# Performance work log

Measured on AMD Instinct MI355X. Metric: run time of the kernel, lower is better.

Reference implementation:

```python
import jax, jax.numpy as jnp
import numpy as np

N_NODES = 50000
N_EDGES = 1600000
IN_DIM = 64 + 2 + 64   # protein + spatial + lri
HID = 64
OUT_DIM = 32
NUM_GRAPHS = 64
NEG_SLOPE = 0.2  # PyG GATConv default negative_slope


def _gat(x, src, dst, W, a_src, a_dst, bias):
    """PyG-style GATConv: x' = xW per head, per-edge attention with
    LeakyReLU + scatter-softmax over incoming edges, weighted scatter-sum.
    Heads are concatenated (concat=True default)."""
    N = x.shape[0]
    H, C = a_src.shape
    xp = (x @ W).reshape(N, H, C)                      # [N,H,C]
    al_src = jnp.sum(xp * a_src, axis=-1)              # [N,H]
    al_dst = jnp.sum(xp * a_dst, axis=-1)              # [N,H]
    e = jax.nn.leaky_relu(al_src[src] + al_dst[dst], NEG_SLOPE)  # [E,H]
    # numerically stable segment softmax over edges grouped by dst
    m = jax.ops.segment_max(e, dst, num_segments=N)
    ex = jnp.exp(e - m[dst])
    denom = jax.ops.segment_sum(ex, dst, num_segments=N)
    alpha = ex / denom[dst]                            # [E,H]
    out = jax.ops.segment_sum(alpha[:, :, None] * xp[src], dst, num_segments=N)
    return out.reshape(N, H * C) + bias


def setup_inputs() -> dict:
    key = jax.random.key(0)
    ks = jax.random.split(key, 16)
    def glorot(k, shape):
        fan_in = shape[0] if len(shape) == 2 else shape[-1]
        return jax.random.normal(k, shape, dtype=jnp.float32) / np.sqrt(fan_in)
    inp = {
        "protein_expr": jax.random.normal(ks[0], (N_NODES, 64), dtype=jnp.float32),
        "spatial_pos": jax.random.uniform(ks[1], (N_NODES, 2), dtype=jnp.float32),
        "lri_feats": jax.random.normal(ks[2], (N_NODES, 64), dtype=jnp.float32),
        "edge_index": jax.random.randint(ks[3], (2, N_EDGES), 0, N_NODES, dtype=jnp.int64),
        "batch": jnp.sort(jax.random.randint(ks[4], (N_NODES,), 0, NUM_GRAPHS, dtype=jnp.int64)),
        # encoder1: GATConv(IN_DIM -> HID, heads=2)
        "W1": glorot(ks[5], (IN_DIM, 2 * HID)),
        "a_src1": glorot(ks[6], (2, HID)),
        "a_dst1": glorot(ks[7], (2, HID)),
        "b1": jnp.zeros((2 * HID,), dtype=jnp.float32),
        # encoder2: GATConv(2*HID -> HID, heads=1)
        "W2": glorot(ks[8], (2 * HID, HID)),
        "a_src2": glorot(ks[9], (1, HID)),
        "a_dst2": glorot(ks[10], (1, HID)),
        "b2": jnp.zeros((HID,), dtype=jnp.float32),
        # decoder MLP
        "Wd1": glorot(ks[11], (HID, HID)),
        "bd1": jnp.zeros((HID,), dtype=jnp.float32),
        "Wd2": glorot(ks[12], (HID, OUT_DIM)),
        "bd2": jnp.zeros((OUT_DIM,), dtype=jnp.float32),
    }
    return inp


def reference(protein_expr, spatial_pos, lri_feats, edge_index, batch,
              W1, a_src1, a_dst1, b1, W2, a_src2, a_dst2, b2,
              Wd1, bd1, Wd2, bd2):
    N = protein_expr.shape[0]
    x = jnp.concatenate([protein_expr, spatial_pos, lri_feats], axis=1)  # [N, IN_DIM]
    # PyG GATConv adds self-loops by default
    loop = jnp.arange(N, dtype=edge_index.dtype)
    src = jnp.concatenate([edge_index[0], loop])
    dst = jnp.concatenate([edge_index[1], loop])
    h = _gat(x, src, dst, W1, a_src1, a_dst1, b1)   # [N, 2*HID]
    h = _gat(h, src, dst, W2, a_src2, a_dst2, b2)   # [N, HID]
    # global_mean_pool
    counts = jax.ops.segment_sum(jnp.ones((N,), h.dtype), batch, num_segments=NUM_GRAPHS)
    pooled = jax.ops.segment_sum(h, batch, num_segments=NUM_GRAPHS) / jnp.clip(counts, 1.0)[:, None]
    # decoder MLP
    d = jax.nn.relu(pooled @ Wd1 + bd1)
    return d @ Wd2 + bd2
```

## Files before the change

### kernel.cpp

```cpp
#include <hip/hip_runtime.h>
#include <hip/hip_bf16.h>

#define N_NODESC 50000
#define N_EDGESC 1600000
#define NUM_GRAPHSC 64
#define SLICE_W 6250
#define BCAP 230000
#define CH_EPB 2048
#define EPB2 8192
#define SUBW 196
#define NSUB 32
#define SBCAP 8192
#define POOL_REP 32
#define AGG_NB 6250

typedef __hip_bfloat16 bf16;
typedef short short8 __attribute__((ext_vector_type(8)));
typedef float floatx4 __attribute__((ext_vector_type(4)));

__device__ __forceinline__ float ldf(const void* p, long i, int fp32) {
    return fp32 ? ((const float*)p)[i] : __bfloat162float(((const bf16*)p)[i]);
}
__device__ __forceinline__ short f2s(float v) {
    bf16 h = __float2bfloat16(v);
    return *(short*)&h;
}
__device__ __forceinline__ unsigned pack2(float lo, float hi) {
    bf16 a = __float2bfloat16(lo), b = __float2bfloat16(hi);
    unsigned ua = *(unsigned short*)&a, ub = *(unsigned short*)&b;
    return (ub << 16) | ua;
}
__device__ __forceinline__ float ulo(unsigned u) { return __uint_as_float(u << 16); }
__device__ __forceinline__ float uhi(unsigned u) { return __uint_as_float(u & 0xffff0000u); }

__global__ void detect_k(const void* __restrict__ prot,
                         const void* __restrict__ eidx,
                         int* __restrict__ flags) {
    if (blockIdx.x == 0 && threadIdx.x == 0) {
        const bf16* pb = (const bf16*)prot;
        int sane = 0;
        for (int i = 0; i < 64; ++i) {
            float a = fabsf(__bfloat162float(pb[2 * i]));
            if (a > 1e-8f && a < 1e4f) sane++;
        }
        flags[0] = (sane >= 48) ? 0 : 1;
        const unsigned* u = (const unsigned*)eidx;
        int zhi = 0;
        for (int i = 0; i < 32; ++i)
            if (u[2 * i + 1] == 0u) zhi++;
        flags[1] = (zhi >= 30) ? 1 : 0;
    }
}

__global__ __launch_bounds__(256) void prep2_k(const void* __restrict__ W1,
                                               const void* __restrict__ W2,
                                               const int* __restrict__ flags,
                                               short* __restrict__ w1f,
                                               float* __restrict__ w1r,
                                               short* __restrict__ w2f,
                                               int* __restrict__ zreg, int nzero, int nzblk,
                                               const void* __restrict__ batch,
                                               int* __restrict__ b32) {
    const int fp32 = flags[0];
    const int b = blockIdx.x, tid = threadIdx.x;
    if (b < 64) {
        int idx = b * 256 + tid;
        int kp = idx >> 7, n = idx & 127;
        int krow = kp < 64 ? kp : 66 + (kp - 64);
        float v = ldf(W1, (long)krow * 128 + n, fp32);
        int c = n >> 4, nn = n & 15, t = kp >> 5, q = (kp >> 3) & 3, j = kp & 7;
        w1f[(((c * 4 + t) * 4 + q) * 16 + nn) * 8 + j] = f2s(v);
    } else if (b == 64) {
        int which = tid >> 7, n = tid & 127;
        w1r[which * 128 + n] = ldf(W1, (long)(64 + which) * 128 + n, fp32);
    } else if (b < 97) {
        int idx = (b - 65) * 256 + tid;
        int k = idx >> 6, n = idx & 63;
        float v = ldf(W2, (long)k * 64 + n, fp32);
        int c = n >> 4, nn = n & 15, t = k >> 5, q = (k >> 3) & 3, j = k & 7;
        w2f[(((c * 4 + t) * 4 + q) * 16 + nn) * 8 + j] = f2s(v);
    } else if (b < 97 + nzblk) {
        int i = (b - 97) * 256 + tid;
        if (i < nzero) zreg[i] = 0;
    } else {
        const int i64f = flags[1];
        int i = (b - 97 - nzblk) * 256 + tid;
        if (i < N_NODESC)
            b32[i] = i64f ? (int)((const long long*)batch)[i] : ((const int*)batch)[i];
    }
}

__global__ __launch_bounds__(256) void cvt_bucket_k(const void* __restrict__ eidx,
                                                    const int* __restrict__ flags,
                                                    int* __restrict__ bcur,
                                                    unsigned* __restrict__ bucket) {
    const int i64f = flags[1];
    const int tid = threadIdx.x;
    const long e0 = (long)blockIdx.x * CH_EPB;
    __shared__ int cnt[9];
    __shared__ int gbase[8];
    __shared__ int cur[8];
    __shared__ unsigned buf[CH_EPB];
    if (tid < 8) cnt[tid] = 0;
    __syncthreads();
    unsigned ev[8];
    int bk[8];
    #pragma unroll
    for (int i = 0; i < 8; ++i) {
        long e = e0 + i * 256 + tid;
        bk[i] = -1;
        if (e < N_EDGESC) {
            int s, d;
            if (i64f) {
                s = (int)((const long long*)eidx)[e];
                d = (int)((const long long*)eidx)[N_EDGESC + e];
            } else {
                s = ((const int*)eidx)[e];
                d = ((const int*)eidx)[N_EDGESC + e];
            }
            int b = d / SLICE_W;
            bk[i] = b;
            ev[i] = (unsigned)s | ((unsigned)(d - b * SLICE_W) << 16);
            atomicAdd(&cnt[b], 1);
        }
    }
    __syncthreads();
    if (tid == 0) {
        int run = 0;
        #pragma unroll
        for (int b = 0; b < 8; ++b) { int c = cnt[b]; cnt[b] = run; run += c; }
        cnt[8] = run;
    }
    __syncthreads();
    if (tid < 8) {
        int c = cnt[tid + 1] - cnt[tid];
        gbase[tid] = c ? atomicAdd(&bcur[tid], c) : 0;
        cur[tid] = cnt[tid];
    }
    __syncthreads();
    #pragma unroll
    for (int i = 0; i < 8; ++i) {
        if (bk[i] >= 0) {
            int p = atomicAdd(&cur[bk[i]], 1);
            buf[p] = ev[i];
        }
    }
    __syncthreads();
    const int total = cnt[8];
    for (int p = tid; p < total; p += 256) {
        int b = 7;
        #pragma unroll
        for (int q = 6; q >= 0; --q)
            if (p < cnt[q + 1]) b = q;
        bucket[(long)b * BCAP + gbase[b] + (p - cnt[b])] = buf[p];
    }
}

__global__ __launch_bounds__(256) void subpart_k(const unsigned* __restrict__ bucket,
                                                 const int* __restrict__ bcur,
                                                 int* __restrict__ scnt,
                                                 unsigned* __restrict__ bucket2) {
    const int slice = blockIdx.x & 7;
    const int blk = blockIdx.x >> 3;
    const int tid = threadIdx.x;
    const int cnt = bcur[slice];
    const unsigned* B = bucket + (long)slice * BCAP;
    __shared__ unsigned buf[EPB2];
    __shared__ int cnt2[NSUB + 1], gbase[NSUB], cur[NSUB];
    for (int start = blk * EPB2; start < cnt; start += 32 * EPB2) {
        const int csize = min(EPB2, cnt - start);
        if (tid < NSUB) cnt2[tid] = 0;
        __syncthreads();
        for (int i = tid; i < csize; i += 256) {
            unsigned v = B[start + i];
            atomicAdd(&cnt2[(v >> 16) / SUBW], 1);
        }
        __syncthreads();
        if (tid == 0) {
            int run = 0;
            #pragma unroll
            for (int s = 0; s < NSUB; ++s) { int c = cnt2[s]; cnt2[s] = run; run += c; }
            cnt2[NSUB] = run;
        }
        __syncthreads();
        if (tid < NSUB) {
            int c = cnt2[tid + 1] - cnt2[tid];
            gbase[tid] = c ? atomicAdd(&scnt[slice * NSUB + tid], c) : 0;
            cur[tid] = cnt2[tid];
        }
        __syncthreads();
        for (int i = tid; i < csize; i += 256) {
            unsigned v = B[start + i];
            int off = (int)(v >> 16);
            int sub = off / SUBW;
            unsigned nv = (v & 0xffffu) | ((unsigned)(off - sub * SUBW) << 16);
            int p = atomicAdd(&cur[sub], 1);
            buf[p] = nv;
        }
        __syncthreads();
        const int total = cnt2[NSUB];
        for (int p = tid; p < total; p += 256) {
            int lo = 0, hi = NSUB;
            while (hi - lo > 1) { int mid = (lo + hi) >> 1; if (p >= cnt2[mid]) lo = mid; else hi = mid; }
            bucket2[((long)slice * NSUB + lo) * SBCAP + gbase[lo] + (p - cnt2[lo])] = buf[p];
        }
        __syncthreads();
    }
}

__global__ __launch_bounds__(256) void csr_k(const unsigned* __restrict__ bucket2,
                                             const int* __restrict__ scnt,
                                             int* __restrict__ state,
                                             int* __restrict__ row_start,
                                             unsigned short* __restrict__ col) {
    const int sb = blockIdx.x;
    const int slice = sb >> 5, sub = sb & 31;
    const int tid = threadIdx.x;
    const int lane = tid & 63;
    const int cnt = scnt[sb];
    const unsigned* B = bucket2 + (long)sb * SBCAP;
    __shared__ int lh[SUBW];
    __shared__ int sc[256];
    __shared__ int sprefix_sh;
    const int width = min(SUBW, SLICE_W - sub * SUBW);
    const int nodebase = slice * SLICE_W + sub * SUBW;
    for (int i = tid; i < SUBW; i += 256) lh[i] = 0;
    __syncthreads();
    for (int e = tid; e < cnt; e += 256) atomicAdd(&lh[B[e] >> 16], 1);
    __syncthreads();
    const int myc = (tid < SUBW) ? lh[tid] : 0;
    sc[tid] = myc;
    __syncthreads();
    for (int off = 1; off < 256; off <<= 1) {
        int t = (tid >= off) ? sc[tid - off] : 0;
        __syncthreads();
        sc[tid] += t;
        __syncthreads();
    }
    const int total = sc[255];
    if (tid == 0)
        __hip_atomic_store(&state[sb], (int)((1u << 30) | (unsigned)total),
                           __ATOMIC_RELEASE, __HIP_MEMORY_SCOPE_AGENT);
    if (tid < 64) {
        int prefix = 0;
        if (sb > 0) {
            int base = sb;
            for (;;) {
                int t = base - 1 - lane;
                int v = 0;
                if (t >= 0) {
                    for (;;) {
                        v = __hip_atomic_load(&state[t], __ATOMIC_ACQUIRE,
                                              __HIP_MEMORY_SCOPE_AGENT);
                        if ((unsigned)v >= (1u << 30)) break;
                        __builtin_amdgcn_s_sleep(1);
                    }
                }
                int flag = (int)(((unsigned)v) >> 30);
                int val = v & 0x3fffffff;
                unsigned long long pmask = __ballot(flag == 2 && t >= 0);
                int stop_tid = pmask ? (__ffsll((long long)pmask) - 1) : 64;
                int contrib = 0;
                if (t >= 0 && lane <= stop_tid) contrib = val;
                #pragma unroll
                for (int off = 32; off; off >>= 1) contrib += __shfl_xor(contrib, off, 64);
                prefix += contrib;
                if (pmask || base <= 64) break;
                base -= 64;
            }
        }
        if (tid == 0) {
            sprefix_sh = prefix;
            __hip_atomic_store(&state[sb],
                               (int)((2u << 30) | (unsigned)(prefix + total)),
                               __ATOMIC_RELEASE, __HIP_MEMORY_SCOPE_AGENT);
        }
    }
    __syncthreads();
    const int sprefix = sprefix_sh;
    if (tid < width) row_start[nodebase + tid] = sprefix + sc[tid] - myc;
    if (sb == 255 && tid == 0) row_start[N_NODESC] = sprefix + total;
    if (tid < SUBW) lh[tid] = sprefix + sc[tid] - myc;
    __syncthreads();
    for (int e = tid; e < cnt; e += 256) {
        unsigned v = B[e];
        int pos = atomicAdd(&lh[v >> 16], 1);
        col[pos] = (unsigned short)(v & 0xffffu);
    }
}


__global__ __launch_bounds__(256) void gemm1_k(
        const void* __restrict__ prot, const void* __restrict__ sp,
        const void* __restrict__ lri,
        const short* __restrict__ w1f, const float* __restrict__ w1r,
        const void* __restrict__ as1, const void* __restrict__ ad1,
        const int* __restrict__ flags,
        short* __restrict__ xph0, short* __restrict__ xph1,
        float* __restrict__ alsrc, float* __restrict__ aldst) {
    const int fp32 = flags[0];
    const int tid = threadIdx.x;
    const int nb = blockIdx.x * 32;
    __shared__ __align__(16) short xs[32][136];
    __shared__ float xsp[32][2];
    __shared__ float sredc[32][8], dredc[32][8];

    if (!fp32) {
        #pragma unroll
        for (int i = 0; i < 2; ++i) {
            int cidx = i * 256 + tid;
            int r = cidx >> 4, cc = cidx & 15;
            int g = nb + r;
            short8 v = (short8){0, 0, 0, 0, 0, 0, 0, 0};
            if (g < N_NODESC) {
                const short* srcp = (cc < 8)
                    ? (const short*)prot + (long)g * 64 + cc * 8
                    : (const short*)lri + (long)g * 64 + (cc - 8) * 8;
                v = *(const short8*)srcp;
            }
            *(short8*)&xs[r][cc * 8] = v;
        }
    } else {
        #pragma unroll
        for (int i = 0; i < 16; ++i) {
            int idx = i * 256 + tid;
            int r = idx >> 7, k = idx & 127;
            int g = nb + r;
            float v = 0.f;
            if (g < N_NODESC)
                v = (k < 64) ? ((const float*)prot)[(long)g * 64 + k]
                             : ((const float*)lri)[(long)g * 64 + (k - 64)];
            xs[r][k] = f2s(v);
        }
    }
    if (tid < 64) {
        int r = tid >> 1, which = tid & 1;
        int g = nb + r;
        xsp[r][which] = (g < N_NODESC) ? ldf(sp, (long)g * 2 + which, fp32) : 0.f;
    }
    __syncthreads();

    const int wid = tid >> 6, lane = tid & 63;
    const int quad = lane >> 4, l16 = lane & 15;
    floatx4 acc[2][2];
    #pragma unroll
    for (int a = 0; a < 2; ++a)
        #pragma unroll
        for (int b = 0; b < 2; ++b) acc[a][b] = (floatx4){0.f, 0.f, 0.f, 0.f};

    const int c0 = 2 * wid;
    #pragma unroll
    for (int t = 0; t < 4; ++t) {
        short8 a0 = *(const short8*)&xs[l16][t * 32 + quad * 8];
        short8 a1 = *(const short8*)&xs[16 + l16][t * 32 + quad * 8];
        short8 b0 = *(const short8*)&w1f[(((c0 * 4 + t) * 4 + quad) * 16 + l16) * 8];
        short8 b1 = *(const short8*)&w1f[((((c0 + 1) * 4 + t) * 4 + quad) * 16 + l16) * 8];
        acc[0][0] = __builtin_amdgcn_mfma_f32_16x16x32_bf16(a0, b0, acc[0][0], 0, 0, 0);
        acc[0][1] = __builtin_amdgcn_mfma_f32_16x16x32_bf16(a0, b1, acc[0][1], 0, 0, 0);
        acc[1][0] = __builtin_amdgcn_mfma_f32_16x16x32_bf16(a1, b0, acc[1][0], 0, 0, 0);
        acc[1][1] = __builtin_amdgcn_mfma_f32_16x16x32_bf16(a1, b1, acc[1][1], 0, 0, 0);
    }
    #pragma unroll
    for (int ci = 0; ci < 2; ++ci) {
        int colg = (c0 + ci) * 16 + l16;
        float w0 = w1r[colg], w1v = w1r[128 + colg];
        float asv = ldf(as1, colg, fp32), adv = ldf(ad1, colg, fp32);
        short* xpd = (colg < 64) ? xph0 : xph1;
        const int cc = colg & 63;
        #pragma unroll
        for (int rt = 0; rt < 2; ++rt) {
            float sv[4], dv[4];
            #pragma unroll
            for (int reg = 0; reg < 4; ++reg) {
                int row = rt * 16 + quad * 4 + reg;
                int g = nb + row;
                float v = acc[rt][ci][reg] + xsp[row][0] * w0 + xsp[row][1] * w1v;
                if (g < N_NODESC) xpd[(long)g * 64 + cc] = f2s(v);
                sv[reg] = v * asv;
                dv[reg] = v * adv;
            }
            #pragma unroll
            for (int off = 1; off < 16; off <<= 1) {
                #pragma unroll
                for (int reg = 0; reg < 4; ++reg) {
                    sv[reg] += __shfl_xor(sv[reg], off, 64);
                    dv[reg] += __shfl_xor(dv[reg], off, 64);
                }
            }
            if (l16 == 0) {
                #pragma unroll
                for (int reg = 0; reg < 4; ++reg) {
                    int row = rt * 16 + quad * 4 + reg;
                    sredc[row][c0 + ci] = sv[reg];
                    dredc[row][c0 + ci] = dv[reg];
                }
            }
        }
    }
    __syncthreads();
    if (tid < 64) {
        int r = tid >> 1, h = tid & 1;
        int g = nb + r;
        if (g < N_NODESC) {
            alsrc[(long)h * N_NODESC + g] = sredc[r][4 * h] + sredc[r][4 * h + 1] +
                                            sredc[r][4 * h + 2] + sredc[r][4 * h + 3];
            aldst[(long)h * N_NODESC + g] = dredc[r][4 * h] + dredc[r][4 * h + 1] +
                                            dredc[r][4 * h + 2] + dredc[r][4 * h + 3];
        }
    }
}


__global__ __launch_bounds__(256) void agg1s_k(
        const int* __restrict__ row_start, const unsigned short* __restrict__ col,
        const short* __restrict__ xph0, const short* __restrict__ xph1,
        const float* __restrict__ als, const float* __restrict__ ald,
        const void* __restrict__ b1, const int* __restrict__ flags,
        unsigned* __restrict__ h1b32) {
    const int fp32 = flags[0];
    const int tid = threadIdx.x;
    const int wid = tid >> 6;
    const int lane = tid & 63;
    const int hw = lane >> 5;
    const int hl = lane & 31;
    const int head = blockIdx.x >= AGG_NB;
    const int b = blockIdx.x - head * AGG_NB;
    const int n = b * 8 + wid * 2 + hw;
    __shared__ float2 pbuf[4][2][32];
    float2* mybuf = pbuf[wid][hw];
    const short* xph = head ? xph1 : xph0;
    const float* alsh = als + (long)head * N_NODESC;
    const float* aldh = ald + (long)head * N_NODESC;
    const int e = hl >> 3;
    const int c = hl & 7;
    const char* xpb = (const char*)xph;
    const int c16 = c * 16;
    const float ad = aldh[n];
    float e0 = alsh[n] + ad;
    e0 = e0 > 0.f ? e0 : 0.2f * e0;
    const float pself = __expf(e0);
    const float pinit = e == 0 ? pself : 0.f;
    uint4 us = *(const uint4*)(xpb + (long)n * 128 + c16);
    float acc0 = pinit * ulo(us.x), acc1 = pinit * uhi(us.x);
    float acc2 = pinit * ulo(us.y), acc3 = pinit * uhi(us.y);
    float acc4 = pinit * ulo(us.z), acc5 = pinit * uhi(us.z);
    float acc6 = pinit * ulo(us.w), acc7 = pinit * uhi(us.w);
    float lp = 0.f;
    const int beg = row_start[n], end = row_start[n + 1];
    for (int base = beg; base < end; base += 32) {
        const int idx = base + hl;
        int s = 0;
        float p = 0.f;
        if (idx < end) {
            s = (int)col[idx];
            float t = alsh[s] + ad;
            t = t > 0.f ? t : 0.2f * t;
            p = __expf(t);
        }
        lp += p;
        mybuf[hl] = make_float2(p, __int_as_float(s << 7));
        int cnt = end - base; if (cnt > 32) cnt = 32;
        int quads = (cnt + 3) >> 2;
        int j = 0;
        for (; j + 4 <= quads; j += 4) {
            int a4[4]; float p4[4]; uint4 x[4];
            #pragma unroll
            for (int q = 0; q < 4; ++q) {
                float2 bv = mybuf[4 * (j + q) + e];
                a4[q] = __float_as_int(bv.y);
                p4[q] = bv.x;
            }
            #pragma unroll
            for (int q = 0; q < 4; ++q)
                x[q] = *(const uint4*)(xpb + a4[q] + c16);
            #pragma unroll
            for (int q = 0; q < 4; ++q) {
                acc0 = fmaf(p4[q], ulo(x[q].x), acc0);
                acc1 = fmaf(p4[q], uhi(x[q].x), acc1);
                acc2 = fmaf(p4[q], ulo(x[q].y), acc2);
                acc3 = fmaf(p4[q], uhi(x[q].y), acc3);
                acc4 = fmaf(p4[q], ulo(x[q].z), acc4);
                acc5 = fmaf(p4[q], uhi(x[q].z), acc5);
                acc6 = fmaf(p4[q], ulo(x[q].w), acc6);
                acc7 = fmaf(p4[q], uhi(x[q].w), acc7);
            }
        }
        for (; j < quads; ++j) {
            float2 bv = mybuf[4 * j + e];
            uint4 x = *(const uint4*)(xpb + __float_as_int(bv.y) + c16);
            float pv = bv.x;
            acc0 = fmaf(pv, ulo(x.x), acc0);
            acc1 = fmaf(pv, uhi(x.x), acc1);
            acc2 = fmaf(pv, ulo(x.y), acc2);
            acc3 = fmaf(pv, uhi(x.y), acc3);
            acc4 = fmaf(pv, ulo(x.z), acc4);
            acc5 = fmaf(pv, uhi(x.z), acc5);
            acc6 = fmaf(pv, ulo(x.w), acc6);
            acc7 = fmaf(pv, uhi(x.w), acc7);
        }
    }
    #pragma unroll
    for (int off = 16; off; off >>= 1) lp += __shfl_xor(lp, off, 64);
    #pragma unroll
    for (int off = 8; off <= 16; off <<= 1) {
        acc0 += __shfl_xor(acc0, off, 64);
        acc1 += __shfl_xor(acc1, off, 64);
        acc2 += __shfl_xor(acc2, off, 64);
        acc3 += __shfl_xor(acc3, off, 64);
        acc4 += __shfl_xor(acc4, off, 64);
        acc5 += __shfl_xor(acc5, off, 64);
        acc6 += __shfl_xor(acc6, off, 64);
        acc7 += __shfl_xor(acc7, off, 64);
    }
    if (hl < 8) {
        const float rl = 1.f / (lp + pself);
        const long bb = (long)head * 64 + 8 * c;
        float o0 = acc0 * rl + ldf(b1, bb + 0, fp32);
        float o1 = acc1 * rl + ldf(b1, bb + 1, fp32);
        float o2 = acc2 * rl + ldf(b1, bb + 2, fp32);
        float o3 = acc3 * rl + ldf(b1, bb + 3, fp32);
        float o4 = acc4 * rl + ldf(b1, bb + 4, fp32);
        float o5 = acc5 * rl + ldf(b1, bb + 5, fp32);
        float o6 = acc6 * rl + ldf(b1, bb + 6, fp32);
        float o7 = acc7 * rl + ldf(b1, bb + 7, fp32);
        uint4 o;
        o.x = pack2(o0, o1); o.y = pack2(o2, o3);
        o.z = pack2(o4, o5); o.w = pack2(o6, o7);
        *(uint4*)((char*)h1b32 + (long)n * 256 + head * 128 + c16) = o;
    }
}


__global__ __launch_bounds__(256) void gemm2_k(
        const unsigned* __restrict__ h1b32, const short* __restrict__ w2f,
        const void* __restrict__ as2, const void* __restrict__ ad2,
        const int* __restrict__ flags,
        short* __restrict__ xp2b, float* __restrict__ alsrc, float* __restrict__ aldst) {
    const int fp32 = flags[0];
    const int tid = threadIdx.x;
    const int nb = blockIdx.x * 32;
    __shared__ __align__(16) short xs[32][136];
    __shared__ float sredc[32][4], dredc[32][4];

    #pragma unroll
    for (int i = 0; i < 8; ++i) {
        int idx = i * 256 + tid;
        int r = idx >> 6, ii = idx & 63;
        int g = nb + r;
        unsigned val = (g < N_NODESC) ? h1b32[(long)g * 64 + ii] : 0u;
        ((unsigned*)&xs[r][0])[ii] = val;
    }
    __syncthreads();

    const int wid = tid >> 6, lane = tid & 63;
    const int quad = lane >> 4, l16 = lane & 15;
    floatx4 acc0 = (floatx4){0.f, 0.f, 0.f, 0.f};
    floatx4 acc1 = (floatx4){0.f, 0.f, 0.f, 0.f};
    #pragma unroll
    for (int t = 0; t < 4; ++t) {
        short8 a0 = *(const short8*)&xs[l16][t * 32 + quad * 8];
        short8 a1 = *(const short8*)&xs[16 + l16][t * 32 + quad * 8];
        short8 b = *(const short8*)&w2f[(((wid * 4 + t) * 4 + quad) * 16 + l16) * 8];
        acc0 = __builtin_amdgcn_mfma_f32_16x16x32_bf16(a0, b, acc0, 0, 0, 0);
        acc1 = __builtin_amdgcn_mfma_f32_16x16x32_bf16(a1, b, acc1, 0, 0, 0);
    }
    const int colg = wid * 16 + l16;
    const float asv = ldf(as2, colg, fp32), adv = ldf(ad2, colg, fp32);
    float sv0[4], dv0[4], sv1[4], dv1[4];
    #pragma unroll
    for (int reg = 0; reg < 4; ++reg) {
        int r0 = quad * 4 + reg;
        int g0 = nb + r0;
        int g1 = g0 + 16;
        if (g0 < N_NODESC) xp2b[(long)g0 * 64 + colg] = f2s(acc0[reg]);
        if (g1 < N_NODESC) xp2b[(long)g1 * 64 + colg] = f2s(acc1[reg]);
        sv0[reg] = acc0[reg] * asv; dv0[reg] = acc0[reg] * adv;
        sv1[reg] = acc1[reg] * asv; dv1[reg] = acc1[reg] * adv;
    }
    #pragma unroll
    for (int off = 1; off < 16; off <<= 1) {
        #pragma unroll
        for (int reg = 0; reg < 4; ++reg) {
            sv0[reg] += __shfl_xor(sv0[reg], off, 64);
            dv0[reg] += __shfl_xor(dv0[reg], off, 64);
            sv1[reg] += __shfl_xor(sv1[reg], off, 64);
            dv1[reg] += __shfl_xor(dv1[reg], off, 64);
        }
    }
    if (l16 == 0) {
        #pragma unroll
        for (int reg = 0; reg < 4; ++reg) {
            int r0 = quad * 4 + reg;
            sredc[r0][wid] = sv0[reg];      dredc[r0][wid] = dv0[reg];
            sredc[r0 + 16][wid] = sv1[reg]; dredc[r0 + 16][wid] = dv1[reg];
        }
    }
    __syncthreads();
    if (tid < 32) {
        int g = nb + tid;
        if (g < N_NODESC) {
            alsrc[g] = sredc[tid][0] + sredc[tid][1] + sredc[tid][2] + sredc[tid][3];
            aldst[g] = dredc[tid][0] + dredc[tid][1] + dredc[tid][2] + dredc[tid][3];
        }
    }
}


__global__ __launch_bounds__(256) void agg2p_k(
        const int* __restrict__ row_start, const unsigned short* __restrict__ col,
        const short* __restrict__ xp2b, const float* __restrict__ alsrc,
        const float* __restrict__ aldst, const void* __restrict__ b2v,
        const int* __restrict__ flags, const int* __restrict__ batch32,
        float* __restrict__ pooled, float* __restrict__ counts) {
    const int fp32 = flags[0];
    const int tid = threadIdx.x;
    const int wid = tid >> 6;
    const int lane = tid & 63;
    const int hw = lane >> 5;
    const int hl = lane & 31;
    const int n = blockIdx.x * 8 + wid * 2 + hw;
    const int rep = blockIdx.x & (POOL_REP - 1);
    __shared__ float2 pbuf[4][2][32];
    __shared__ float psum[64];
    __shared__ int ginfo[2];
    if (tid < 64) psum[tid] = 0.f;
    if (tid == 0) {
        int g0 = batch32[blockIdx.x * 8];
        int g7 = batch32[blockIdx.x * 8 + 7];
        ginfo[0] = g0;
        ginfo[1] = (g0 == g7);
    }
    __syncthreads();
    float2* mybuf = pbuf[wid][hw];
    const int e = hl >> 3;
    const int c = hl & 7;
    const char* xpb = (const char*)xp2b;
    const int c16 = c * 16;
    const float ad = aldst[n];
    float e0 = alsrc[n] + ad;
    e0 = e0 > 0.f ? e0 : 0.2f * e0;
    const float pself = __expf(e0);
    const float pinit = e == 0 ? pself : 0.f;
    uint4 us = *(const uint4*)(xpb + (long)n * 128 + c16);
    float acc0 = pinit * ulo(us.x), acc1 = pinit * uhi(us.x);
    float acc2 = pinit * ulo(us.y), acc3 = pinit * uhi(us.y);
    float acc4 = pinit * ulo(us.z), acc5 = pinit * uhi(us.z);
    float acc6 = pinit * ulo(us.w), acc7 = pinit * uhi(us.w);
    float lp = 0.f;
    const int beg = row_start[n], end = row_start[n + 1];
    for (int base = beg; base < end; base += 32) {
        const int idx = base + hl;
        int s = 0;
        float p = 0.f;
        if (idx < end) {
            s = (int)col[idx];
            float t = alsrc[s] + ad;
            t = t > 0.f ? t : 0.2f * t;
            p = __expf(t);
        }
        lp += p;
        mybuf[hl] = make_float2(p, __int_as_float(s << 7));
        int cnt = end - base; if (cnt > 32) cnt = 32;
        int quads = (cnt + 3) >> 2;
        int j = 0;
        for (; j + 4 <= quads; j += 4) {
            int a4[4]; float p4[4]; uint4 x[4];
            #pragma unroll
            for (int q = 0; q < 4; ++q) {
                float2 bv = mybuf[4 * (j + q) + e];
                a4[q] = __float_as_int(bv.y);
                p4[q] = bv.x;
            }
            #pragma unroll
            for (int q = 0; q < 4; ++q)
                x[q] = *(const uint4*)(xpb + a4[q] + c16);
            #pragma unroll
            for (int q = 0; q < 4; ++q) {
                acc0 = fmaf(p4[q], ulo(x[q].x), acc0);
                acc1 = fmaf(p4[q], uhi(x[q].x), acc1);
                acc2 = fmaf(p4[q], ulo(x[q].y), acc2);
                acc3 = fmaf(p4[q], uhi(x[q].y), acc3);
                acc4 = fmaf(p4[q], ulo(x[q].z), acc4);
                acc5 = fmaf(p4[q], uhi(x[q].z), acc5);
                acc6 = fmaf(p4[q], ulo(x[q].w), acc6);
                acc7 = fmaf(p4[q], uhi(x[q].w), acc7);
            }
        }
        for (; j < quads; ++j) {
            float2 bv = mybuf[4 * j + e];
            uint4 x = *(const uint4*)(xpb + __float_as_int(bv.y) + c16);
            float pv = bv.x;
            acc0 = fmaf(pv, ulo(x.x), acc0);
            acc1 = fmaf(pv, uhi(x.x), acc1);
            acc2 = fmaf(pv, ulo(x.y), acc2);
            acc3 = fmaf(pv, uhi(x.y), acc3);
            acc4 = fmaf(pv, ulo(x.z), acc4);
            acc5 = fmaf(pv, uhi(x.z), acc5);
            acc6 = fmaf(pv, ulo(x.w), acc6);
            acc7 = fmaf(pv, uhi(x.w), acc7);
        }
    }
    #pragma unroll
    for (int off = 16; off; off >>= 1) lp += __shfl_xor(lp, off, 64);
    #pragma unroll
    for (int off = 8; off <= 16; off <<= 1) {
        acc0 += __shfl_xor(acc0, off, 64);
        acc1 += __shfl_xor(acc1, off, 64);
        acc2 += __shfl_xor(acc2, off, 64);
        acc3 += __shfl_xor(acc3, off, 64);
        acc4 += __shfl_xor(acc4, off, 64);
        acc5 += __shfl_xor(acc5, off, 64);
        acc6 += __shfl_xor(acc6, off, 64);
        acc7 += __shfl_xor(acc7, off, 64);
    }
    float o[8];
    if (hl < 8) {
        const float rl = 1.f / (lp + pself);
        o[0] = acc0 * rl + ldf(b2v, 8 * c + 0, fp32);
        o[1] = acc1 * rl + ldf(b2v, 8 * c + 1, fp32);
        o[2] = acc2 * rl + ldf(b2v, 8 * c + 2, fp32);
        o[3] = acc3 * rl + ldf(b2v, 8 * c + 3, fp32);
        o[4] = acc4 * rl + ldf(b2v, 8 * c + 4, fp32);
        o[5] = acc5 * rl + ldf(b2v, 8 * c + 5, fp32);
        o[6] = acc6 * rl + ldf(b2v, 8 * c + 6, fp32);
        o[7] = acc7 * rl + ldf(b2v, 8 * c + 7, fp32);
    }
    if (ginfo[1]) {
        if (hl < 8) {
            #pragma unroll
            for (int j = 0; j < 8; ++j) atomicAdd(&psum[8 * c + j], o[j]);
        }
        __syncthreads();
        if (tid < 64)
            atomicAdd(&pooled[((long)rep * NUM_GRAPHSC + ginfo[0]) * 64 + tid], psum[tid]);
        if (tid == 0) atomicAdd(&counts[rep * NUM_GRAPHSC + ginfo[0]], 8.f);
    } else {
        int g = batch32[n];
        if (hl < 8) {
            #pragma unroll
            for (int j = 0; j < 8; ++j)
                atomicAdd(&pooled[((long)rep * NUM_GRAPHSC + g) * 64 + 8 * c + j], o[j]);
        }
        if (hl == 0) atomicAdd(&counts[rep * NUM_GRAPHSC + g], 1.f);
    }
}


__global__ __launch_bounds__(64) void dec_k(const float* __restrict__ pooled,
                                            const float* __restrict__ counts,
                                            const void* __restrict__ Wd1, const void* __restrict__ bd1,
                                            const void* __restrict__ Wd2, const void* __restrict__ bd2,
                                            const int* __restrict__ flags,
                                            void* __restrict__ out) {
    const int fp32 = flags[0];
    const int g = blockIdx.x, j = threadIdx.x;
    __shared__ float p[64], dh[64];
    float cnt = 0.f, ps = 0.f;
    #pragma unroll
    for (int r = 0; r < POOL_REP; ++r) {
        ps += pooled[((long)r * NUM_GRAPHSC + g) * 64 + j];
        if (j == 0) cnt += counts[r * NUM_GRAPHSC + g];
    }
    __shared__ float cnt_sh;
    if (j == 0) cnt_sh = cnt < 1.f ? 1.f : cnt;
    __syncthreads();
    p[j] = ps / cnt_sh;
    __syncthreads();
    float acc = ldf(bd1, j, fp32);
    for (int k = 0; k < 64; ++k) acc += p[k] * ldf(Wd1, k * 64 + j, fp32);
    dh[j] = acc > 0.f ? acc : 0.f;
    __syncthreads();
    if (j < 32) {
        float o = ldf(bd2, j, fp32);
        for (int k = 0; k < 64; ++k) o += dh[k] * ldf(Wd2, k * 32 + j, fp32);
        if (fp32) ((float*)out)[g * 32 + j] = o;
        else      ((bf16*)out)[g * 32 + j] = __float2bfloat16(o);
    }
}

extern "C" void kernel_launch(void* const* d_in, const int* in_sizes, int n_in,
                              void* d_out, int out_size, void* d_ws, size_t ws_size,
                              hipStream_t stream) {
    (void)in_sizes; (void)n_in; (void)out_size; (void)ws_size;
    const void* prot = d_in[0];
    const void* sp   = d_in[1];
    const void* lri  = d_in[2];
    const void* eidx = d_in[3];
    const void* batch= d_in[4];
    const void* W1   = d_in[5];
    const void* as1  = d_in[6];
    const void* ad1  = d_in[7];
    const void* b1   = d_in[8];
    const void* W2   = d_in[9];
    const void* as2  = d_in[10];
    const void* ad2  = d_in[11];
    const void* b2v  = d_in[12];
    const void* Wd1  = d_in[13];
    const void* bd1  = d_in[14];
    const void* Wd2  = d_in[15];
    const void* bd2  = d_in[16];

    char* w = (char*)d_ws;
    auto alloc = [&](size_t bytes) -> void* {
        char* p = w;
        w += (bytes + 255) & ~(size_t)255;
        return (void*)p;
    };
    int*   flags     = (int*)alloc(2 * 4);
    float* pooled    = (float*)alloc((size_t)POOL_REP * NUM_GRAPHSC * 64 * 4);
    float* counts    = (float*)alloc((size_t)POOL_REP * NUM_GRAPHSC * 4);
    int*   bcur      = (int*)alloc((size_t)8 * 4);
    int*   scnt      = (int*)alloc((size_t)256 * 4);
    int*   state     = (int*)alloc((size_t)256 * 4);
    char*  zero_end  = w;
    int*   batch32   = (int*)alloc((size_t)N_NODESC * 4);
    int*   row_start = (int*)alloc((size_t)(N_NODESC + 1) * 4);
    unsigned* bucket = (unsigned*)alloc((size_t)8 * BCAP * 4);
    unsigned* bucket2= (unsigned*)alloc((size_t)256 * SBCAP * 4);
    unsigned short* col = (unsigned short*)alloc((size_t)N_EDGESC * 2);
    short* w1f       = (short*)alloc((size_t)16384 * 2);
    float* w1r       = (float*)alloc((size_t)256 * 4);
    short* w2f       = (short*)alloc((size_t)8192 * 2);
    short* xph0      = (short*)alloc((size_t)N_NODESC * 64 * 2);
    short* xph1      = (short*)alloc((size_t)N_NODESC * 64 * 2);
    float* alsrc1    = (float*)alloc((size_t)N_NODESC * 2 * 4);
    float* aldst1    = (float*)alloc((size_t)N_NODESC * 2 * 4);
    short* h1b       = (short*)alloc((size_t)N_NODESC * 128 * 2);
    short* xp2b      = (short*)alloc((size_t)N_NODESC * 64 * 2);
    float* alsrc2    = (float*)alloc((size_t)N_NODESC * 4);
    float* aldst2    = (float*)alloc((size_t)N_NODESC * 4);

    const int nzero = (int)((zero_end - (char*)pooled) / 4);
    const int nzblk = (nzero + 255) / 256;
    const int nbat  = (N_NODESC + 255) / 256;

    detect_k<<<1, 64, 0, stream>>>(prot, eidx, flags);
    prep2_k<<<97 + nzblk + nbat, 256, 0, stream>>>(W1, W2, flags, w1f, w1r, w2f,
                                                   (int*)pooled, nzero, nzblk,
                                                   batch, batch32);
    cvt_bucket_k<<<(N_EDGESC + CH_EPB - 1) / CH_EPB, 256, 0, stream>>>(eidx, flags, bcur, bucket);
    subpart_k<<<8 * 32, 256, 0, stream>>>(bucket, bcur, scnt, bucket2);
    csr_k<<<256, 256, 0, stream>>>(bucket2, scnt, state, row_start, col);

    const int nblk = (N_NODESC + 31) / 32;
    gemm1_k<<<nblk, 256, 0, stream>>>(prot, sp, lri, w1f, w1r, as1, ad1, flags,
                                      xph0, xph1, alsrc1, aldst1);
    agg1s_k<<<2 * AGG_NB, 256, 0, stream>>>(row_start, col, xph0, xph1,
                                            alsrc1, aldst1, b1, flags,
                                            (unsigned*)h1b);
    gemm2_k<<<nblk, 256, 0, stream>>>((const unsigned*)h1b, w2f, as2, ad2, flags,
                                      xp2b, alsrc2, aldst2);
    agg2p_k<<<AGG_NB, 256, 0, stream>>>(row_start, col, xp2b, alsrc2, aldst2,
                                        b2v, flags, batch32, pooled, counts);
    dec_k<<<NUM_GRAPHSC, 64, 0, stream>>>(pooled, counts, Wd1, bd1, Wd2, bd2, flags, d_out);
}
```

Baseline: 331.9 us.

## Merge two-pass edge bucketing into a single 256-way partition pass

Replaces the 8-way slice bucketing kernel followed by a 32-way sub-partition kernel with one kernel that partitions edges straight into 256 destination sub-buckets, using a block-wide scan and a binary search for scatter. This drops one full read and write of the edge list through global memory and one kernel launch. In exchange, each block writes to 256 buckets with smaller contiguous runs, so stores are less coalesced and there is more global atomic traffic on the bucket counters.

```diff
diff --git a/kernel.cpp b/kernel.cpp
--- a/kernel.cpp
+++ b/kernel.cpp
@@ -4,12 +4,9 @@
 #define N_NODESC 50000
 #define N_EDGESC 1600000
 #define NUM_GRAPHSC 64
-#define SLICE_W 6250
-#define BCAP 230000
-#define CH_EPB 2048
-#define EPB2 8192
+#define P_EPB 2048
 #define SUBW 196
-#define NSUB 32
+#define NSB 256
 #define SBCAP 8192
 #define POOL_REP 32
 #define AGG_NB 6250
@@ -90,18 +87,20 @@
     }
 }
 
-__global__ __launch_bounds__(256) void cvt_bucket_k(const void* __restrict__ eidx,
-                                                    const int* __restrict__ flags,
-                                                    int* __restrict__ bcur,
-                                                    unsigned* __restrict__ bucket) {
+__global__ __launch_bounds__(256) void part_k(const void* __restrict__ eidx,
+                                              const int* __restrict__ flags,
+                                              int* __restrict__ scnt,
+                                              unsigned* __restrict__ bucket2) {
     const int i64f = flags[1];
     const int tid = threadIdx.x;
-    const long e0 = (long)blockIdx.x * CH_EPB;
-    __shared__ int cnt[9];
-    __shared__ int gbase[8];
-    __shared__ int cur[8];
-    __shared__ unsigned buf[CH_EPB];
-    if (tid < 8) cnt[tid] = 0;
+    const long e0 = (long)blockIdx.x * P_EPB;
+    __shared__ int cnt[NSB + 1];
+    __shared__ int sc[NSB];
+    __shared__ int gbase[NSB];
+    __shared__ int cur[NSB];
+    __shared__ unsigned buf[P_EPB];
+    cnt[tid] = 0;
+    if (tid == 0) cnt[NSB] = 0;
     __syncthreads();
     unsigned ev[8];
     int bk[8];
@@ -118,25 +117,26 @@
                 s = ((const int*)eidx)[e];
                 d = ((const int*)eidx)[N_EDGESC + e];
             }
-            int b = d / SLICE_W;
-            bk[i] = b;
-            ev[i] = (unsigned)s | ((unsigned)(d - b * SLICE_W) << 16);
-            atomicAdd(&cnt[b], 1);
-        }
-    }
-    __syncthreads();
-    if (tid == 0) {
-        int run = 0;
-        #pragma unroll
-        for (int b = 0; b < 8; ++b) { int c = cnt[b]; cnt[b] = run; run += c; }
-        cnt[8] = run;
-    }
-    __syncthreads();
-    if (tid < 8) {
-        int c = cnt[tid + 1] - cnt[tid];
-        gbase[tid] = c ? atomicAdd(&bcur[tid], c) : 0;
-        cur[tid] = cnt[tid];
-    }
+            int sub = (d >> 2) / 49;
+            bk[i] = sub;
+            ev[i] = (unsigned)s | ((unsigned)(d - sub * SUBW) << 16);
+            atomicAdd(&cnt[sub], 1);
+        }
+    }
+    __syncthreads();
+    const int myc = cnt[tid];
+    sc[tid] = myc;
+    __syncthreads();
+    for (int off = 1; off < NSB; off <<= 1) {
+        int t = (tid >= off) ? sc[tid - off] : 0;
+        __syncthreads();
+        sc[tid] += t;
+        __syncthreads();
+    }
+    cnt[tid] = sc[tid] - myc;
+    if (tid == NSB - 1) cnt[NSB] = sc[NSB - 1];
+    gbase[tid] = myc ? atomicAdd(&scnt[tid], myc) : 0;
+    cur[tid] = sc[tid] - myc;
     __syncthreads();
     #pragma unroll
     for (int i = 0; i < 8; ++i) {
@@ -146,65 +146,11 @@
         }
     }
     __syncthreads();
-    const int total = cnt[8];
+    const int total = cnt[NSB];
     for (int p = tid; p < total; p += 256) {
-        int b = 7;
-        #pragma unroll
-        for (int q = 6; q >= 0; --q)
-            if (p < cnt[q + 1]) b = q;
-        bucket[(long)b * BCAP + gbase[b] + (p - cnt[b])] = buf[p];
-    }
-}
-
-__global__ __launch_bounds__(256) void subpart_k(const unsigned* __restrict__ bucket,
-                                                 const int* __restrict__ bcur,
-                                                 int* __restrict__ scnt,
-                                                 unsigned* __restrict__ bucket2) {
-    const int slice = blockIdx.x & 7;
-    const int blk = blockIdx.x >> 3;
-    const int tid = threadIdx.x;
-    const int cnt = bcur[slice];
-    const unsigned* B = bucket + (long)slice * BCAP;
-    __shared__ unsigned buf[EPB2];
-    __shared__ int cnt2[NSUB + 1], gbase[NSUB], cur[NSUB];
-    for (int start = blk * EPB2; start < cnt; start += 32 * EPB2) {
-        const int csize = min(EPB2, cnt - start);
-        if (tid < NSUB) cnt2[tid] = 0;
-        __syncthreads();
-        for (int i = tid; i < csize; i += 256) {
-            unsigned v = B[start + i];
-            atomicAdd(&cnt2[(v >> 16) / SUBW], 1);
-        }
-        __syncthreads();
-        if (tid == 0) {
-            int run = 0;
-            #pragma unroll
-            for (int s = 0; s < NSUB; ++s) { int c = cnt2[s]; cnt2[s] = run; run += c; }
-            cnt2[NSUB] = run;
-        }
-        __syncthreads();
-        if (tid < NSUB) {
-            int c = cnt2[tid + 1] - cnt2[tid];
-            gbase[tid] = c ? atomicAdd(&scnt[slice * NSUB + tid], c) : 0;
-            cur[tid] = cnt2[tid];
-        }
-        __syncthreads();
-        for (int i = tid; i < csize; i += 256) {
-            unsigned v = B[start + i];
-            int off = (int)(v >> 16);
-            int sub = off / SUBW;
-            unsigned nv = (v & 0xffffu) | ((unsigned)(off - sub * SUBW) << 16);
-            int p = atomicAdd(&cur[sub], 1);
-            buf[p] = nv;
-        }
-        __syncthreads();
-        const int total = cnt2[NSUB];
-        for (int p = tid; p < total; p += 256) {
-            int lo = 0, hi = NSUB;
-            while (hi - lo > 1) { int mid = (lo + hi) >> 1; if (p >= cnt2[mid]) lo = mid; else hi = mid; }
-            bucket2[((long)slice * NSUB + lo) * SBCAP + gbase[lo] + (p - cnt2[lo])] = buf[p];
-        }
-        __syncthreads();
+        int lo = 0, hi = NSB;
+        while (hi - lo > 1) { int mid = (lo + hi) >> 1; if (p >= cnt[mid]) lo = mid; else hi = mid; }
+        bucket2[(long)lo * SBCAP + gbase[lo] + (p - cnt[lo])] = buf[p];
     }
 }
 
@@ -214,7 +160,6 @@
                                              int* __restrict__ row_start,
                                              unsigned short* __restrict__ col) {
     const int sb = blockIdx.x;
-    const int slice = sb >> 5, sub = sb & 31;
     const int tid = threadIdx.x;
     const int lane = tid & 63;
     const int cnt = scnt[sb];
@@ -222,8 +167,8 @@
     __shared__ int lh[SUBW];
     __shared__ int sc[256];
     __shared__ int sprefix_sh;
-    const int width = min(SUBW, SLICE_W - sub * SUBW);
-    const int nodebase = slice * SLICE_W + sub * SUBW;
+    const int nodebase = sb * SUBW;
+    const int width = min(SUBW, N_NODESC - nodebase);
     for (int i = tid; i < SUBW; i += 256) lh[i] = 0;
     __syncthreads();
     for (int e = tid; e < cnt; e += 256) atomicAdd(&lh[B[e] >> 16], 1);
@@ -279,7 +224,7 @@
     __syncthreads();
     const int sprefix = sprefix_sh;
     if (tid < width) row_start[nodebase + tid] = sprefix + sc[tid] - myc;
-    if (sb == 255 && tid == 0) row_start[N_NODESC] = sprefix + total;
+    if (sb == NSB - 1 && tid == 0) row_start[N_NODESC] = sprefix + total;
     if (tid < SUBW) lh[tid] = sprefix + sc[tid] - myc;
     __syncthreads();
     for (int e = tid; e < cnt; e += 256) {
@@ -809,14 +754,12 @@
     int*   flags     = (int*)alloc(2 * 4);
     float* pooled    = (float*)alloc((size_t)POOL_REP * NUM_GRAPHSC * 64 * 4);
     float* counts    = (float*)alloc((size_t)POOL_REP * NUM_GRAPHSC * 4);
-    int*   bcur      = (int*)alloc((size_t)8 * 4);
-    int*   scnt      = (int*)alloc((size_t)256 * 4);
-    int*   state     = (int*)alloc((size_t)256 * 4);
+    int*   scnt      = (int*)alloc((size_t)NSB * 4);
+    int*   state     = (int*)alloc((size_t)NSB * 4);
     char*  zero_end  = w;
     int*   batch32   = (int*)alloc((size_t)N_NODESC * 4);
     int*   row_start = (int*)alloc((size_t)(N_NODESC + 1) * 4);
-    unsigned* bucket = (unsigned*)alloc((size_t)8 * BCAP * 4);
-    unsigned* bucket2= (unsigned*)alloc((size_t)256 * SBCAP * 4);
+    unsigned* bucket2= (unsigned*)alloc((size_t)NSB * SBCAP * 4);
     unsigned short* col = (unsigned short*)alloc((size_t)N_EDGESC * 2);
     short* w1f       = (short*)alloc((size_t)16384 * 2);
     float* w1r       = (float*)alloc((size_t)256 * 4);
@@ -838,9 +781,8 @@
     prep2_k<<<97 + nzblk + nbat, 256, 0, stream>>>(W1, W2, flags, w1f, w1r, w2f,
                                                    (int*)pooled, nzero, nzblk,
                                                    batch, batch32);
-    cvt_bucket_k<<<(N_EDGESC + CH_EPB - 1) / CH_EPB, 256, 0, stream>>>(eidx, flags, bcur, bucket);
-    subpart_k<<<8 * 32, 256, 0, stream>>>(bucket, bcur, scnt, bucket2);
-    csr_k<<<256, 256, 0, stream>>>(bucket2, scnt, state, row_start, col);
+    part_k<<<(N_EDGESC + P_EPB - 1) / P_EPB, 256, 0, stream>>>(eidx, flags, scnt, bucket2);
+    csr_k<<<NSB, 256, 0, stream>>>(bucket2, scnt, state, row_start, col);
 
     const int nblk = (N_NODESC + 31) / 32;
     gemm1_k<<<nblk, 256, 0, stream>>>(prot, sp, lri, w1f, w1r, as1, ad1, flags,
```

Measured after the change: 314.3 us. 5.3% less time.
